# Kernel tuning notes

Measured on AMD Instinct MI355X. Metric: run time of the kernel, lower is better.

Reference implementation:

```python
import jax, jax.numpy as jnp
import numpy as np

VOCAB, D, K = 100000, 300, 5

def setup_inputs() -> dict:
    key = jax.random.key(0)
    ks = jax.random.split(key, 12)
    B, BAG, L = 64, 16, 128
    token_ids = jax.random.randint(ks[0], (B * BAG, L), 0, VOCAB)
    mention_rep = jax.random.normal(ks[1], (B, BAG, D), dtype=jnp.float32)
    s = 0.05
    emb = jax.random.normal(ks[2], (VOCAB, D), dtype=jnp.float32)
    W1 = jax.random.normal(ks[3], (D, D), dtype=jnp.float32) * s
    b1 = jnp.zeros((D,), jnp.float32)
    conv_w = jax.random.normal(ks[4], (D, D, K), dtype=jnp.float32) * s  # [out, in, k]
    conv_b = jnp.zeros((D,), jnp.float32)
    W2 = jax.random.normal(ks[5], (2 * D, D), dtype=jnp.float32) * s
    b2 = jnp.zeros((D,), jnp.float32)
    W3 = jax.random.normal(ks[6], (D, D), dtype=jnp.float32) * s
    b3 = jnp.zeros((D,), jnp.float32)
    return {"token_ids": token_ids, "mention_rep": mention_rep, "emb": emb,
            "W1": W1, "b1": b1, "conv_w": conv_w, "conv_b": conv_b,
            "W2": W2, "b2": b2, "W3": W3, "b3": b3}

def reference(token_ids, mention_rep, emb, W1, b1, conv_w, conv_b, W2, b2, W3, b3):
    # fused gather+pad: [N, L, D]
    x = emb[token_ids]
    # lin1
    x = x @ W1 + b1
    # conv1d over time, VALID, stride 1: NCH layout
    xc = jnp.transpose(x, (0, 2, 1))  # [N, D, L]
    y = jax.lax.conv_general_dilated(xc, conv_w, (1,), 'VALID',
                                     dimension_numbers=('NCH', 'OIH', 'NCH'))
    y = y + conv_b[None, :, None]
    cnn_out = jnp.max(y, axis=-1)  # [N, D]
    m = mention_rep.reshape(mention_rep.shape[0] * mention_rep.shape[1], -1)  # dropout = identity (eval)
    concat = jnp.concatenate([cnn_out, m], axis=-1)
    h = jnp.tanh(concat @ W2 + b2)
    out = h @ W3 + b3  # dropout = identity (eval)
    return out
```

## Files before the change

### kernel.cpp

```cpp
#include <hip/hip_runtime.h>


#define DD   300
#define LL   128
#define TOUT 124
#define CH   16
#define XR   20
#define NSTG 8
#define BLK  320
#define KS     19
#define SLABP  6080
#define ROWP   20
#define WS_G1_OFF  0
#define WS_CV_OFF  194560
#define WS_NEEDED  1167360
#define NPH        114

typedef __attribute__((ext_vector_type(8))) _Float16 f16x8;
typedef __attribute__((ext_vector_type(4))) _Float16 f16x4;
typedef __attribute__((ext_vector_type(4))) float f32x4;
typedef __attribute__((ext_vector_type(16))) float f32x16;
typedef unsigned int   u32;
typedef unsigned short u16;
typedef __attribute__((ext_vector_type(4))) u32 u32x4;

__device__ __forceinline__ float b2f(u16 u) {
    union { float f; u32 i; } x; x.i = ((u32)u) << 16; return x.f;
}
__device__ __forceinline__ u16 f2bu(float f) {
    union { float f; u32 i; } x; x.f = f;
    u32 r = x.i + 0x7FFFu + ((x.i >> 16) & 1u);
    return (u16)(r >> 16);
}
__device__ __forceinline__ float ld(const void* p, size_t idx, int is32) {
    return is32 ? ((const float*)p)[idx] : b2f(((const u16*)p)[idx]);
}
__device__ __forceinline__ int sniff_is32(const void* W1) {
    int cnt = 0;
    const u32* w1raw = (const u32*)W1;
    for (int i = 0; i < 64; ++i) {
        u32 e = (w1raw[i] >> 7) & 0xFFu;
        cnt += (e >= 100u && e <= 126u) ? 1 : 0;
    }
    return (cnt < 32) ? 1 : 0;
}

__device__ __forceinline__ void barrier_lgkm() {
    asm volatile("s_waitcnt lgkmcnt(0)" ::: "memory");
    __builtin_amdgcn_s_barrier();
}

__device__ __forceinline__ void unit_decomp(int u, int& o, int& kq) {
    kq = (u >= 912) ? 3 : (u >= 608) ? 2 : (u >= 304) ? 1 : 0;
    o  = u - 304 * kq;
}
__device__ __forceinline__ void g1_load(const float* W1f, int kk, int o, int kq, float r[4]) {
    const int kbase = kk * 16 + kq * 4;
    #pragma unroll
    for (int j = 0; j < 4; ++j) {
        const int k = kbase + j;
        r[j] = (k < DD && o < DD) ? W1f[(size_t)k * DD + o] : 0.f;
    }
}
__device__ __forceinline__ void g1_write(_Float16* Ws, int o, int kq, const float r[4]) {
    f16x4 v;
    #pragma unroll
    for (int j = 0; j < 4; ++j) v[j] = (_Float16)r[j];
    *(f16x4*)&Ws[o * ROWP + (kq << 2)] = v;
}
__device__ __forceinline__ void cv_load(const float* CWf, int kk, int o, int kq, float r[20]) {
    const int kbase = kk * 16 + kq * 4;
    const bool ok = (o < DD) && (kbase < DD);
    const float4* src = (const float4*)(CWf + (size_t)o * 1500 + kk * 80 + kq * 20);
    #pragma unroll
    for (int i = 0; i < 5; ++i) {
        float4 t = ok ? src[i] : float4{0.f, 0.f, 0.f, 0.f};
        r[4*i] = t.x; r[4*i+1] = t.y; r[4*i+2] = t.z; r[4*i+3] = t.w;
    }
}
__device__ __forceinline__ void cv_write(_Float16* Ws, int o, int kq, const float r[20]) {
    #pragma unroll
    for (int s = 0; s < 5; ++s) {
        f16x4 v;
        #pragma unroll
        for (int j = 0; j < 4; ++j) v[j] = (_Float16)r[j * 5 + s];
        *(f16x4*)&Ws[s * SLABP + o * ROWP + (kq << 2)] = v;
    }
}

__global__ void CNNEncoder_36258113912977_xform(
    const void* W1, const void* conv_w, void* ws)
{
    if (!sniff_is32(W1)) return;
    const int kk = blockIdx.x, part = blockIdx.y, tid = threadIdx.x;

    if (part == 0) {
        const float* W1f = (const float*)W1;
        f16x8* dst = (f16x8*)((char*)ws + WS_G1_OFF) + (size_t)kk * 640;
        for (int g = tid; g < 640; g += 512) {
            const int kc = (g >= 320) ? 1 : 0;
            const int nn = g - kc * 320;
            f16x8 v;
            #pragma unroll
            for (int e = 0; e < 8; ++e) {
                const int k = kk * 16 + kc * 8 + e;
                v[e] = (_Float16)((k < DD && nn < DD) ? W1f[(size_t)k * DD + nn] : 0.f);
            }
            dst[g] = v;
        }
    } else {
        const int s = part - 1;
        const float* CWf = (const float*)conv_w;
        f16x8* dst = (f16x8*)((char*)ws + WS_CV_OFF) + (size_t)kk * 3200 + (size_t)s * 640;
        for (int g = tid; g < 640; g += 512) {
            const int kc = (g >= 320) ? 1 : 0;
            const int nn = g - kc * 320;
            f16x8 v;
            #pragma unroll
            for (int e = 0; e < 8; ++e) {
                const int k = kk * 16 + kc * 8 + e;
                v[e] = (_Float16)((k < DD && nn < DD)
                        ? CWf[(size_t)nn * 1500 + (size_t)k * 5 + s] : 0.f);
            }
            dst[g] = v;
        }
    }
}

#define STAGE_PH(P, Q, QX) do {                                             \
    const int wr_ = (P) + 5;                                                \
    if (wr_ < NPH) {                                                        \
        _Float16* d_ = &ring[(wr_ % 6) * 5120];                             \
        *(u32x4*)&d_[tid * 8] = Q;                                          \
        if (tid < 128) *(u32x4*)&d_[(512 + tid) * 8] = QX;                  \
    }                                                                       \
    const int lp_ = (P) + 7;                                                \
    if (lp_ < NPH) {                                                        \
        const u32x4* s_ = (const u32x4*)wsAll + (size_t)lp_ * 640;          \
        Q = s_[tid];                                                        \
        if (tid < 128) QX = s_[512 + tid];                                  \
    }                                                                       \
} while (0)

#define PH_BODY(P, SROW, KKC, Q, QX) do {                                   \
    STAGE_PH((P), Q, QX);                                                   \
    const int phys_ = (P) % 6;                                              \
    const int c_ = 2 * (KKC) + lh;                                          \
    const int row_ = mrow0 + l31 + (SROW);                                  \
    const f16x8 a_ = *(const f16x8*)&XB[row_ * 320 + ((c_ ^ (row_ & 7)) << 3)]; \
    __builtin_amdgcn_s_setprio(1);                                          \
    _Pragma("unroll")                                                       \
    for (int nt_ = 0; nt_ < 5; ++nt_) {                                     \
        const int nn_ = nbase + nt_ * 32 + l31;                             \
        const f16x8 b_ = *(const f16x8*)&ring[phys_ * 5120 + lh * 2560 + nn_ * 8]; \
        acc[nt_] = __builtin_amdgcn_mfma_f32_32x32x16_f16(a_, b_, acc[nt_], 0, 0, 0); \
    }                                                                       \
    __builtin_amdgcn_s_setprio(0);                                          \
    barrier_lgkm();                                                         \
} while (0)

#define PH_G1(KK, Q, QX)    PH_BODY((KK), 0, (KK), Q, QX)
#define PH_CV(KK, S, Q, QX) PH_BODY(19 + (KK) * 5 + (S), (S), (KK), Q, QX)

__global__ __launch_bounds__(512, 2) void CNNEncoder_36258113912977_kernel(
    const int* __restrict__ tok, const void* mention, const void* emb,
    const void* W1, const void* b1, const void* conv_w, const void* conv_b,
    const void* W2, const void* b2, const void* W3, const void* b3,
    void* out, const void* ws)
{
    if (!sniff_is32(W1)) return;

    __shared__ __align__(16) _Float16 XB[132 * 320];
    __shared__ __align__(16) _Float16 ring[6 * 5120];
    __shared__ float pmax4[4][320];
    __shared__ float cbuf[2 * DD];
    __shared__ float hbuf[DD];

    const int n = blockIdx.x, tid = threadIdx.x;
    const int w   = tid >> 6;
    const int l   = tid & 63;
    const int l31 = l & 31, lh = l >> 5;
    const int wm  = w >> 1;
    const int wn  = w & 1;
    const int nbase = wn * 160;
    const int mrow0 = wm * 32;
    const int* trow = tok + (size_t)n * LL;
    const void* wsAll = ws;

    u32x4 qE, qO, qEx, qOx;
    u32x4 pre[5], prex[5];

    #pragma unroll
    for (int pl = 0; pl < 5; ++pl) {
        const u32x4* s_ = (const u32x4*)wsAll + (size_t)pl * 640;
        pre[pl] = s_[tid];
        if (tid < 128) prex[pl] = s_[512 + tid];
    }
    { const u32x4* s_ = (const u32x4*)wsAll + (size_t)5 * 640;
      qE = s_[tid]; if (tid < 128) qEx = s_[512 + tid]; }
    { const u32x4* s_ = (const u32x4*)wsAll + (size_t)6 * 640;
      qO = s_[tid]; if (tid < 128) qOx = s_[512 + tid]; }

    for (int i = tid; i < 132 * 160; i += 512) ((u32*)XB)[i] = 0u;
    __syncthreads();

    {
        const int r = tid >> 2, q = tid & 3;
        const float* erow = (const float*)emb + (size_t)trow[r] * DD;
        for (int c = q; c < 38; c += 4) {
            f16x8 v;
            if (c < 37) {
                const float4 f0 = *(const float4*)(erow + 8 * c);
                const float4 f1 = *(const float4*)(erow + 8 * c + 4);
                v[0]=(_Float16)f0.x; v[1]=(_Float16)f0.y;
                v[2]=(_Float16)f0.z; v[3]=(_Float16)f0.w;
                v[4]=(_Float16)f1.x; v[5]=(_Float16)f1.y;
                v[6]=(_Float16)f1.z; v[7]=(_Float16)f1.w;
            } else {
                const float4 f0 = *(const float4*)(erow + 296);
                v[0]=(_Float16)f0.x; v[1]=(_Float16)f0.y;
                v[2]=(_Float16)f0.z; v[3]=(_Float16)f0.w;
                v[4]=(_Float16)0.f; v[5]=(_Float16)0.f;
                v[6]=(_Float16)0.f; v[7]=(_Float16)0.f;
            }
            const int p = c ^ (r & 7);
            *(f16x8*)&XB[r * 320 + (p << 3)] = v;
        }
    }

    #pragma unroll
    for (int pl = 0; pl < 5; ++pl) {
        *(u32x4*)&ring[pl * 5120 + tid * 8] = pre[pl];
        if (tid < 128) *(u32x4*)&ring[pl * 5120 + (512 + tid) * 8] = prex[pl];
    }
    __syncthreads();

    f32x16 acc[5];
    #pragma unroll
    for (int nt = 0; nt < 5; ++nt)
        #pragma unroll
        for (int j = 0; j < 16; ++j) acc[nt][j] = 0.f;

    for (int kk = 0; kk < 18; kk += 2) {
        PH_G1(kk,     qE, qEx);
        PH_G1(kk + 1, qO, qOx);
    }
    PH_G1(18, qE, qEx);

    {
        const float* b1f = (const float*)b1;
        #pragma unroll
        for (int nt = 0; nt < 5; ++nt) {
            const int col = nbase + nt * 32 + l31;
            const float bb = (col < DD) ? b1f[col] : 0.f;
            const int cc = col >> 3, c7 = col & 7;
            #pragma unroll
            for (int q = 0; q < 4; ++q) {
                #pragma unroll
                for (int r = 0; r < 4; ++r) {
                    const int row = mrow0 + q * 8 + 4 * lh + r;
                    XB[row * 320 + ((cc ^ (row & 7)) << 3) + c7]
                        = (_Float16)(acc[nt][4 * q + r] + bb);
                }
            }
        }
    }
    __syncthreads();

    #pragma unroll
    for (int nt = 0; nt < 5; ++nt)
        #pragma unroll
        for (int j = 0; j < 16; ++j) acc[nt][j] = 0.f;

    for (int kk = 0; kk < 18; kk += 2) {
        PH_CV(kk, 0, qO, qOx);  PH_CV(kk, 1, qE, qEx);
        PH_CV(kk, 2, qO, qOx);  PH_CV(kk, 3, qE, qEx);
        PH_CV(kk, 4, qO, qOx);
        PH_CV(kk + 1, 0, qE, qEx);  PH_CV(kk + 1, 1, qO, qOx);
        PH_CV(kk + 1, 2, qE, qEx);  PH_CV(kk + 1, 3, qO, qOx);
        PH_CV(kk + 1, 4, qE, qEx);
    }
    PH_CV(18, 0, qO, qOx);  PH_CV(18, 1, qE, qEx);
    PH_CV(18, 2, qO, qOx);  PH_CV(18, 3, qE, qEx);
    PH_CV(18, 4, qO, qOx);

    #pragma unroll
    for (int nt = 0; nt < 5; ++nt) {
        float m = -3.0e38f;
        #pragma unroll
        for (int q = 0; q < 4; ++q) {
            if (!(wm == 3 && q == 3)) {
                #pragma unroll
                for (int r = 0; r < 4; ++r) m = fmaxf(m, acc[nt][4 * q + r]);
            } else if (lh == 0) {
                #pragma unroll
                for (int r = 0; r < 4; ++r) m = fmaxf(m, acc[nt][12 + r]);
            }
        }
        m = fmaxf(m, __shfl_xor(m, 32));
        if (lh == 0) pmax4[wm][nbase + nt * 32 + l31] = m;
    }
    __syncthreads();

    if (tid < DD) {
        float m = fmaxf(fmaxf(pmax4[0][tid], pmax4[1][tid]),
                        fmaxf(pmax4[2][tid], pmax4[3][tid]));
        cbuf[tid]      = m + ((const float*)conv_b)[tid];
        cbuf[DD + tid] = ((const float*)mention)[(size_t)n * DD + tid];
    }
    __syncthreads();

    if (tid < DD) {
        const float* W2f = (const float*)W2;
        float a0 = 0.f, a1 = 0.f, a2 = 0.f, a3 = 0.f;
        for (int c = 0; c < 2 * DD; c += 4) {
            a0 += cbuf[c]     * W2f[(size_t)c * DD + tid];
            a1 += cbuf[c + 1] * W2f[(size_t)(c + 1) * DD + tid];
            a2 += cbuf[c + 2] * W2f[(size_t)(c + 2) * DD + tid];
            a3 += cbuf[c + 3] * W2f[(size_t)(c + 3) * DD + tid];
        }
        hbuf[tid] = tanhf(((const float*)b2)[tid] + (a0 + a1) + (a2 + a3));
    }
    __syncthreads();

    if (tid < DD) {
        const float* W3f = (const float*)W3;
        float a0 = 0.f, a1 = 0.f;
        for (int c = 0; c < DD; c += 2) {
            a0 += hbuf[c]     * W3f[(size_t)c * DD + tid];
            a1 += hbuf[c + 1] * W3f[(size_t)(c + 1) * DD + tid];
        }
        ((float*)out)[(size_t)n * DD + tid] = ((const float*)b3)[tid] + a0 + a1;
    }
}

__global__ __launch_bounds__(512, 2) void CNNEncoder_36258113912977_nows(
    const int* __restrict__ tok, const void* mention, const void* emb,
    const void* W1, const void* b1, const void* conv_w, const void* conv_b,
    const void* W2, const void* b2, const void* W3, const void* b3,
    void* out)
{
    if (!sniff_is32(W1)) return;

    __shared__ __align__(16) _Float16 XB[132 * 320];
    __shared__ __align__(16) _Float16 Ws[5 * SLABP];
    __shared__ float pmax2[2][304];
    __shared__ float cbuf[2 * DD];
    __shared__ float hbuf[DD];

    const int n = blockIdx.x, tid = threadIdx.x;
    const int w   = tid >> 6;
    const int l   = tid & 63;
    const int l15 = l & 15, lg = l >> 4;
    const int wm  = w >> 2;
    const int wn  = w & 3;
    const int ntw   = (wn < 3) ? 5 : 4;
    const int nbase = wn * 80;
    const int mrow0 = wm * 64;
    const int* trow = tok + (size_t)n * LL;
    const float* W1f = (const float*)W1;
    const float* CWf = (const float*)conv_w;

    int o0, kq0, o1, kq1, o2, kq2;
    unit_decomp(tid, o0, kq0);
    unit_decomp(512 + tid, o1, kq1);
    const bool act2 = (l < 24);
    unit_decomp(1024 + w * 24 + (l < 24 ? l : 0), o2, kq2);

    for (int i = tid; i < 132 * 160; i += 512) ((u32*)XB)[i] = 0u;
    __syncthreads();

    {
        const int r = tid >> 2, q = tid & 3;
        const float* erow = (const float*)emb + (size_t)trow[r] * DD;
        for (int c = q; c < 38; c += 4) {
            f16x8 v;
            if (c < 37) {
                const float4 f0 = *(const float4*)(erow + 8 * c);
                const float4 f1 = *(const float4*)(erow + 8 * c + 4);
                v[0]=(_Float16)f0.x; v[1]=(_Float16)f0.y;
                v[2]=(_Float16)f0.z; v[3]=(_Float16)f0.w;
                v[4]=(_Float16)f1.x; v[5]=(_Float16)f1.y;
                v[6]=(_Float16)f1.z; v[7]=(_Float16)f1.w;
            } else {
                const float4 f0 = *(const float4*)(erow + 296);
                v[0]=(_Float16)f0.x; v[1]=(_Float16)f0.y;
                v[2]=(_Float16)f0.z; v[3]=(_Float16)f0.w;
                v[4]=(_Float16)0.f; v[5]=(_Float16)0.f;
                v[6]=(_Float16)0.f; v[7]=(_Float16)0.f;
            }
            const int p = c ^ (r & 7);
            *(f16x8*)&XB[r * 320 + (p << 3)] = v;
        }
    }

    f32x4 acc[4][5];
    const f32x4 vzero = {0.f, 0.f, 0.f, 0.f};
    #pragma unroll
    for (int mt = 0; mt < 4; ++mt)
        #pragma unroll
        for (int nt = 0; nt < 5; ++nt) acc[mt][nt] = vzero;

    float g1a[4], g1b[4], g1c[4];
    float cfa[20], cfb[20], cfc[20];

    g1_load(W1f, 0, o0, kq0, g1a);
    g1_load(W1f, 0, o1, kq1, g1b);
    if (act2) g1_load(W1f, 0, o2, kq2, g1c);
    __syncthreads();

    for (int kk = 0; kk < KS; ++kk) {
        g1_write(Ws, o0, kq0, g1a);
        g1_write(Ws, o1, kq1, g1b);
        if (act2) g1_write(Ws, o2, kq2, g1c);
        barrier_lgkm();
        if (kk + 1 < KS) {
            g1_load(W1f, kk + 1, o0, kq0, g1a);
            g1_load(W1f, kk + 1, o1, kq1, g1b);
            if (act2) g1_load(W1f, kk + 1, o2, kq2, g1c);
        } else {
            cv_load(CWf, 0, o0, kq0, cfa);
            cv_load(CWf, 0, o1, kq1, cfb);
            if (act2) cv_load(CWf, 0, o2, kq2, cfc);
        }
        {
            f16x4 af[4];
            #pragma unroll
            for (int mt = 0; mt < 4; ++mt) {
                const int row = mrow0 + mt * 16 + l15;
                const int c = (kk << 1) + (lg >> 1);
                af[mt] = *(const f16x4*)&XB[row * 320 + ((c ^ (row & 7)) << 3) + ((lg & 1) << 2)];
            }
            #pragma unroll
            for (int nt = 0; nt < 5; ++nt) {
                if (nt < ntw) {
                    const int nn = nbase + nt * 16 + l15;
                    const f16x4 b = *(const f16x4*)&Ws[nn * ROWP + (lg << 2)];
                    #pragma unroll
                    for (int mt = 0; mt < 4; ++mt)
                        acc[mt][nt] = __builtin_amdgcn_mfma_f32_16x16x16f16(af[mt], b, acc[mt][nt], 0, 0, 0);
                }
            }
        }
        __builtin_amdgcn_s_barrier();
    }

    {
        const float* b1f = (const float*)b1;
        #pragma unroll
        for (int nt = 0; nt < 5; ++nt) {
            if (nt < ntw) {
                const int col = nbase + nt * 16 + l15;
                const float bb = (col < DD) ? b1f[col] : 0.f;
                #pragma unroll
                for (int mt = 0; mt < 4; ++mt) {
                    #pragma unroll
                    for (int j = 0; j < 4; ++j) {
                        const int row = mrow0 + mt * 16 + (lg << 2) + j;
                        XB[row * 320 + (((col >> 3) ^ (row & 7)) << 3) + (col & 7)]
                            = (_Float16)(acc[mt][nt][j] + bb);
                    }
                }
            }
        }
    }

    #pragma unroll
    for (int mt = 0; mt < 4; ++mt)
        #pragma unroll
        for (int nt = 0; nt < 5; ++nt) acc[mt][nt] = vzero;

    for (int kk = 0; kk < KS; ++kk) {
        cv_write(Ws, o0, kq0, cfa);
        cv_write(Ws, o1, kq1, cfb);
        if (act2) cv_write(Ws, o2, kq2, cfc);
        barrier_lgkm();
        if (kk + 1 < KS) {
            cv_load(CWf, kk + 1, o0, kq0, cfa);
            cv_load(CWf, kk + 1, o1, kq1, cfb);
            if (act2) cv_load(CWf, kk + 1, o2, kq2, cfc);
        }
        #pragma unroll
        for (int s = 0; s < 5; ++s) {
            f16x4 af[4];
            #pragma unroll
            for (int mt = 0; mt < 4; ++mt) {
                const int row = mrow0 + mt * 16 + l15 + s;
                const int c = (kk << 1) + (lg >> 1);
                af[mt] = *(const f16x4*)&XB[row * 320 + ((c ^ (row & 7)) << 3) + ((lg & 1) << 2)];
            }
            #pragma unroll
            for (int nt = 0; nt < 5; ++nt) {
                if (nt < ntw) {
                    const int nn = nbase + nt * 16 + l15;
                    const f16x4 b = *(const f16x4*)&Ws[s * SLABP + nn * ROWP + (lg << 2)];
                    #pragma unroll
                    for (int mt = 0; mt < 4; ++mt)
                        acc[mt][nt] = __builtin_amdgcn_mfma_f32_16x16x16f16(af[mt], b, acc[mt][nt], 0, 0, 0);
                }
            }
        }
        __builtin_amdgcn_s_barrier();
    }

    #pragma unroll
    for (int nt = 0; nt < 5; ++nt) {
        if (nt < ntw) {
            float m = -3.0e38f;
            #pragma unroll
            for (int mt = 0; mt < 4; ++mt) {
                #pragma unroll
                for (int j = 0; j < 4; ++j) {
                    const int t = mrow0 + mt * 16 + (lg << 2) + j;
                    if (t < TOUT) m = fmaxf(m, acc[mt][nt][j]);
                }
            }
            m = fmaxf(m, __shfl_xor(m, 16));
            m = fmaxf(m, __shfl_xor(m, 32));
            if (lg == 0) pmax2[wm][nbase + nt * 16 + l15] = m;
        }
    }
    __syncthreads();

    if (tid < DD) {
        const float m = fmaxf(pmax2[0][tid], pmax2[1][tid]);
        cbuf[tid]      = m + ((const float*)conv_b)[tid];
        cbuf[DD + tid] = ((const float*)mention)[(size_t)n * DD + tid];
    }
    __syncthreads();

    if (tid < DD) {
        const float* W2f = (const float*)W2;
        float a0 = 0.f, a1 = 0.f, a2 = 0.f, a3 = 0.f;
        for (int c = 0; c < 2 * DD; c += 4) {
            a0 += cbuf[c]     * W2f[(size_t)c * DD + tid];
            a1 += cbuf[c + 1] * W2f[(size_t)(c + 1) * DD + tid];
            a2 += cbuf[c + 2] * W2f[(size_t)(c + 2) * DD + tid];
            a3 += cbuf[c + 3] * W2f[(size_t)(c + 3) * DD + tid];
        }
        hbuf[tid] = tanhf(((const float*)b2)[tid] + (a0 + a1) + (a2 + a3));
    }
    __syncthreads();

    if (tid < DD) {
        const float* W3f = (const float*)W3;
        float a0 = 0.f, a1 = 0.f;
        for (int c = 0; c < DD; c += 2) {
            a0 += hbuf[c]     * W3f[(size_t)c * DD + tid];
            a1 += hbuf[c + 1] * W3f[(size_t)(c + 1) * DD + tid];
        }
        ((float*)out)[(size_t)n * DD + tid] = ((const float*)b3)[tid] + a0 + a1;
    }
}

__global__ void CNNEncoder_36258113912977_fallback(
    const int* tok, const void* mention, const void* emb,
    const void* W1, const void* b1, const void* conv_w, const void* conv_b,
    const void* W2, const void* b2, const void* W3, const void* b3,
    void* out)
{
    __shared__ float g[XR * DD];
    __shared__ float xh[XR * DD];
    __shared__ float concat[2 * DD];
    __shared__ float hbuf[DD];

    const int n = blockIdx.x, tid = threadIdx.x;
    const int* trow = tok + (size_t)n * LL;

    if (sniff_is32(W1)) return;
    const int is32 = 0;

    float mmax = -3.0e38f;

    for (int stage = 0; stage < NSTG; ++stage) {
        const int tbase = stage * CH;
        __syncthreads();

        for (int i = tid; i < XR * DD; i += BLK) {
            int r = i / DD, c = i - (i / DD) * DD;
            int gr = tbase + r; if (gr > 127) gr = 127;
            g[i] = ld(emb, (size_t)trow[gr] * DD + c, is32);
        }
        __syncthreads();

        if (tid < DD) {
            float acc[XR];
            #pragma unroll
            for (int r = 0; r < XR; ++r) acc[r] = 0.f;
            for (int k = 0; k < DD; ++k) {
                float wv = ld(W1, (size_t)k * DD + tid, is32);
                #pragma unroll
                for (int r = 0; r < XR; ++r) acc[r] += g[r * DD + k] * wv;
            }
            float bb = ld(b1, tid, is32);
            #pragma unroll
            for (int r = 0; r < XR; ++r) xh[r * DD + tid] = acc[r] + bb;
        }
        __syncthreads();

        if (tid < DD) {
            float y[CH];
            #pragma unroll
            for (int t = 0; t < CH; ++t) y[t] = 0.f;
            const size_t cwoff = (size_t)tid * (DD * 5);
            for (int k = 0; k < DD; ++k) {
                #pragma unroll
                for (int s = 0; s < 5; ++s) {
                    float wv = ld(conv_w, cwoff + k * 5 + s, is32);
                    #pragma unroll
                    for (int t = 0; t < CH; ++t)
                        y[t] += xh[(t + s) * DD + k] * wv;
                }
            }
            #pragma unroll
            for (int t = 0; t < CH; ++t) {
                int tt = tbase + t;
                if (tt < TOUT) mmax = fmaxf(mmax, y[t]);
            }
        }
    }

    __syncthreads();
    if (tid < DD) {
        concat[tid]      = mmax + ld(conv_b, tid, is32);
        concat[DD + tid] = ld(mention, (size_t)n * DD + tid, is32);
    }
    __syncthreads();

    if (tid < DD) {
        float a = ld(b2, tid, is32);
        for (int c = 0; c < 2 * DD; ++c)
            a += concat[c] * ld(W2, (size_t)c * DD + tid, is32);
        hbuf[tid] = tanhf(a);
    }
    __syncthreads();

    if (tid < DD) {
        float a = ld(b3, tid, is32);
        for (int c = 0; c < DD; ++c)
            a += hbuf[c] * ld(W3, (size_t)c * DD + tid, is32);
        ((u16*)out)[(size_t)n * DD + tid] = f2bu(a);
    }
}

extern "C" void kernel_launch(void* const* d_in, const int* in_sizes, int n_in,
                              void* d_out, int out_size, void* d_ws, size_t ws_size,
                              hipStream_t stream)
{
    if (ws_size >= (size_t)WS_NEEDED && d_ws != nullptr) {
        CNNEncoder_36258113912977_xform<<<dim3(19, 6), 512, 0, stream>>>(
            d_in[3], d_in[5], d_ws);
        CNNEncoder_36258113912977_kernel<<<1024, 512, 0, stream>>>(
            (const int*)d_in[0], d_in[1], d_in[2], d_in[3], d_in[4], d_in[5],
            d_in[6], d_in[7], d_in[8], d_in[9], d_in[10], d_out, d_ws);
    } else {
        CNNEncoder_36258113912977_nows<<<1024, 512, 0, stream>>>(
            (const int*)d_in[0], d_in[1], d_in[2], d_in[3], d_in[4], d_in[5],
            d_in[6], d_in[7], d_in[8], d_in[9], d_in[10], d_out);
    }
    CNNEncoder_36258113912977_fallback<<<1024, BLK, 0, stream>>>(
        (const int*)d_in[0], d_in[1], d_in[2], d_in[3], d_in[4], d_in[5],
        d_in[6], d_in[7], d_in[8], d_in[9], d_in[10], d_out);
}
```

Before: 466.7 us.

## Double main kernel block to 1024 threads, splitting MFMA N-tiles across 16 waves

Each block of the main fused kernel now runs 16 waves instead of 8. Each wave owns two or three 32-wide N tiles instead of five, and ten waves together stage one full 640-vector weight phase into the LDS ring with one load each, so the extra tail loads are gone. The W2 and W3 epilogue matvecs are split into two partial sums over 600 threads and combined through a new shared buffer. The aim is more latency hiding and MFMA issue parallelism per CU while LDS limits residency to one block. The cost is lower per-wave accumulator reuse of the A operand, and a tighter register budget under the new launch bounds that may cause spills.

```diff
diff --git a/kernel.cpp b/kernel.cpp
--- a/kernel.cpp
+++ b/kernel.cpp
@@ -127,42 +127,65 @@
     }
 }
 
-#define STAGE_PH(P, Q, QX) do {                                             \
-    const int wr_ = (P) + 5;                                                \
-    if (wr_ < NPH) {                                                        \
-        _Float16* d_ = &ring[(wr_ % 6) * 5120];                             \
-        *(u32x4*)&d_[tid * 8] = Q;                                          \
-        if (tid < 128) *(u32x4*)&d_[(512 + tid) * 8] = QX;                  \
-    }                                                                       \
-    const int lp_ = (P) + 7;                                                \
-    if (lp_ < NPH) {                                                        \
-        const u32x4* s_ = (const u32x4*)wsAll + (size_t)lp_ * 640;          \
-        Q = s_[tid];                                                        \
-        if (tid < 128) QX = s_[512 + tid];                                  \
+#define STAGE_PH(P, Q) do {                                                 \
+    if (stager) {                                                           \
+        const int wr_ = (P) + 5;                                            \
+        if (wr_ < NPH) *(u32x4*)&ring[(wr_ % 6) * 5120 + sg * 8] = Q;       \
+        const int lp_ = (P) + 7;                                            \
+        if (lp_ < NPH) Q = ((const u32x4*)ws)[(size_t)lp_ * 640 + sg];      \
     }                                                                       \
 } while (0)
 
-#define PH_BODY(P, SROW, KKC, Q, QX) do {                                   \
-    STAGE_PH((P), Q, QX);                                                   \
-    const int phys_ = (P) % 6;                                              \
+#define PH_BODY(P, SROW, KKC, Q) do {                                       \
+    STAGE_PH((P), Q);                                                       \
     const int c_ = 2 * (KKC) + lh;                                          \
     const int row_ = mrow0 + l31 + (SROW);                                  \
     const f16x8 a_ = *(const f16x8*)&XB[row_ * 320 + ((c_ ^ (row_ & 7)) << 3)]; \
+    const _Float16* bp_ = &ring[((P) % 6) * 5120 + lh * 2560];              \
     __builtin_amdgcn_s_setprio(1);                                          \
-    _Pragma("unroll")                                                       \
-    for (int nt_ = 0; nt_ < 5; ++nt_) {                                     \
-        const int nn_ = nbase + nt_ * 32 + l31;                             \
-        const f16x8 b_ = *(const f16x8*)&ring[phys_ * 5120 + lh * 2560 + nn_ * 8]; \
-        acc[nt_] = __builtin_amdgcn_mfma_f32_32x32x16_f16(a_, b_, acc[nt_], 0, 0, 0); \
-    }                                                                       \
+    { const f16x8 b_ = *(const f16x8*)&bp_[nn0 * 8];                        \
+      acc0 = __builtin_amdgcn_mfma_f32_32x32x16_f16(a_, b_, acc0, 0, 0, 0); } \
+    { const f16x8 b_ = *(const f16x8*)&bp_[nn1 * 8];                        \
+      acc1 = __builtin_amdgcn_mfma_f32_32x32x16_f16(a_, b_, acc1, 0, 0, 0); } \
+    if (nt3) { const f16x8 b_ = *(const f16x8*)&bp_[nn2 * 8];               \
+      acc2 = __builtin_amdgcn_mfma_f32_32x32x16_f16(a_, b_, acc2, 0, 0, 0); } \
     __builtin_amdgcn_s_setprio(0);                                          \
     barrier_lgkm();                                                         \
 } while (0)
 
-#define PH_G1(KK, Q, QX)    PH_BODY((KK), 0, (KK), Q, QX)
-#define PH_CV(KK, S, Q, QX) PH_BODY(19 + (KK) * 5 + (S), (S), (KK), Q, QX)
-
-__global__ __launch_bounds__(512, 2) void CNNEncoder_36258113912977_kernel(
+#define PH_G1(KK, Q)    PH_BODY((KK), 0, (KK), Q)
+#define PH_CV(KK, S, Q) PH_BODY(19 + (KK) * 5 + (S), (S), (KK), Q)
+
+#define EPI_TILE(ACC, TILE) do {                                            \
+    const int col_ = (TILE) * 32 + l31;                                     \
+    const float bb_ = (col_ < DD) ? b1f[col_] : 0.f;                        \
+    const int cc_ = col_ >> 3, c7_ = col_ & 7;                              \
+    _Pragma("unroll")                                                       \
+    for (int q_ = 0; q_ < 4; ++q_) {                                        \
+        _Pragma("unroll")                                                   \
+        for (int r_ = 0; r_ < 4; ++r_) {                                    \
+            const int row_ = mrow0 + q_ * 8 + 4 * lh + r_;                  \
+            XB[row_ * 320 + ((cc_ ^ (row_ & 7)) << 3) + c7_]                \
+                = (_Float16)(ACC[4 * q_ + r_] + bb_);                       \
+        } }                                                                 \
+} while (0)
+
+#define MAX_TILE(ACC, TILE) do {                                            \
+    float m_ = -3.0e38f;                                                    \
+    _Pragma("unroll")                                                       \
+    for (int q_ = 0; q_ < 4; ++q_) {                                        \
+        if (!(wm == 3 && q_ == 3)) {                                        \
+            _Pragma("unroll")                                               \
+            for (int r_ = 0; r_ < 4; ++r_) m_ = fmaxf(m_, ACC[4 * q_ + r_]); \
+        } else if (lh == 0) {                                               \
+            _Pragma("unroll")                                               \
+            for (int r_ = 0; r_ < 4; ++r_) m_ = fmaxf(m_, ACC[12 + r_]);    \
+        } }                                                                 \
+    m_ = fmaxf(m_, __shfl_xor(m_, 32));                                     \
+    if (lh == 0) pmax4[wm][(TILE) * 32 + l31] = m_;                         \
+} while (0)
+
+__global__ __launch_bounds__(1024, 4) void CNNEncoder_36258113912977_kernel(
     const int* __restrict__ tok, const void* mention, const void* emb,
     const void* W1, const void* b1, const void* conv_w, const void* conv_b,
     const void* W2, const void* b2, const void* W3, const void* b3,
@@ -174,32 +197,187 @@
     __shared__ __align__(16) _Float16 ring[6 * 5120];
     __shared__ float pmax4[4][320];
     __shared__ float cbuf[2 * DD];
+    __shared__ float hpart[2][DD];
     __shared__ float hbuf[DD];
 
     const int n = blockIdx.x, tid = threadIdx.x;
     const int w   = tid >> 6;
     const int l   = tid & 63;
     const int l31 = l & 31, lh = l >> 5;
-    const int wm  = w >> 1;
-    const int wn  = w & 1;
-    const int nbase = wn * 160;
+    const int wm  = w >> 2;
+    const int wn  = w & 3;
     const int mrow0 = wm * 32;
+    const bool nt3 = (wn < 2);
+    const int nn0 = wn * 32 + l31;
+    const int nn1 = nn0 + 128;
+    const int nn2 = nn0 + 256;
+    const bool stager = (w < 10);
+    const int sg = w * 64 + l;
     const int* trow = tok + (size_t)n * LL;
-    const void* wsAll = ws;
-
-    u32x4 qE, qO, qEx, qOx;
-    u32x4 pre[5], prex[5];
-
-    #pragma unroll
-    for (int pl = 0; pl < 5; ++pl) {
-        const u32x4* s_ = (const u32x4*)wsAll + (size_t)pl * 640;
-        pre[pl] = s_[tid];
-        if (tid < 128) prex[pl] = s_[512 + tid];
-    }
-    { const u32x4* s_ = (const u32x4*)wsAll + (size_t)5 * 640;
-      qE = s_[tid]; if (tid < 128) qEx = s_[512 + tid]; }
-    { const u32x4* s_ = (const u32x4*)wsAll + (size_t)6 * 640;
-      qO = s_[tid]; if (tid < 128) qOx = s_[512 + tid]; }
+
+    u32x4 qE, qO;
+    u32x4 pre0, pre1, pre2, pre3, pre4;
+
+    if (stager) {
+        const u32x4* wsv = (const u32x4*)ws;
+        pre0 = wsv[sg];          pre1 = wsv[640 + sg];
+        pre2 = wsv[1280 + sg];   pre3 = wsv[1920 + sg];
+        pre4 = wsv[2560 + sg];
+        qE   = wsv[3200 + sg];
+        qO   = wsv[3840 + sg];
+    }
+
+    for (int i = tid; i < 132 * 160; i += 1024) ((u32*)XB)[i] = 0u;
+    barrier_lgkm();
+
+    {
+        const int r = tid >> 3, q = tid & 7;
+        const float* erow = (const float*)emb + (size_t)trow[r] * DD;
+        for (int c = q; c < 38; c += 8) {
+            f16x8 v;
+            if (c < 37) {
+                const float4 f0 = *(const float4*)(erow + 8 * c);
+                const float4 f1 = *(const float4*)(erow + 8 * c + 4);
+                v[0]=(_Float16)f0.x; v[1]=(_Float16)f0.y;
+                v[2]=(_Float16)f0.z; v[3]=(_Float16)f0.w;
+                v[4]=(_Float16)f1.x; v[5]=(_Float16)f1.y;
+                v[6]=(_Float16)f1.z; v[7]=(_Float16)f1.w;
+            } else {
+                const float4 f0 = *(const float4*)(erow + 296);
+                v[0]=(_Float16)f0.x; v[1]=(_Float16)f0.y;
+                v[2]=(_Float16)f0.z; v[3]=(_Float16)f0.w;
+                v[4]=(_Float16)0.f; v[5]=(_Float16)0.f;
+                v[6]=(_Float16)0.f; v[7]=(_Float16)0.f;
+            }
+            const int p = c ^ (r & 7);
+            *(f16x8*)&XB[r * 320 + (p << 3)] = v;
+        }
+    }
+
+    if (stager) {
+        *(u32x4*)&ring[0 * 5120 + sg * 8] = pre0;
+        *(u32x4*)&ring[1 * 5120 + sg * 8] = pre1;
+        *(u32x4*)&ring[2 * 5120 + sg * 8] = pre2;
+        *(u32x4*)&ring[3 * 5120 + sg * 8] = pre3;
+        *(u32x4*)&ring[4 * 5120 + sg * 8] = pre4;
+    }
+    barrier_lgkm();
+
+    f32x16 acc0, acc1, acc2;
+    #pragma unroll
+    for (int j = 0; j < 16; ++j) { acc0[j] = 0.f; acc1[j] = 0.f; acc2[j] = 0.f; }
+
+    for (int kk = 0; kk < 18; kk += 2) {
+        PH_G1(kk,     qE);
+        PH_G1(kk + 1, qO);
+    }
+    PH_G1(18, qE);
+
+    {
+        const float* b1f = (const float*)b1;
+        EPI_TILE(acc0, wn);
+        EPI_TILE(acc1, wn + 4);
+        if (nt3) EPI_TILE(acc2, wn + 8);
+    }
+    barrier_lgkm();
+
+    #pragma unroll
+    for (int j = 0; j < 16; ++j) { acc0[j] = 0.f; acc1[j] = 0.f; acc2[j] = 0.f; }
+
+    for (int kk = 0; kk < 18; kk += 2) {
+        PH_CV(kk, 0, qO);  PH_CV(kk, 1, qE);
+        PH_CV(kk, 2, qO);  PH_CV(kk, 3, qE);
+        PH_CV(kk, 4, qO);
+        PH_CV(kk + 1, 0, qE);  PH_CV(kk + 1, 1, qO);
+        PH_CV(kk + 1, 2, qE);  PH_CV(kk + 1, 3, qO);
+        PH_CV(kk + 1, 4, qE);
+    }
+    PH_CV(18, 0, qO);  PH_CV(18, 1, qE);
+    PH_CV(18, 2, qO);  PH_CV(18, 3, qE);
+    PH_CV(18, 4, qO);
+
+    MAX_TILE(acc0, wn);
+    MAX_TILE(acc1, wn + 4);
+    if (nt3) MAX_TILE(acc2, wn + 8);
+    __syncthreads();
+
+    if (tid < DD) {
+        float m = fmaxf(fmaxf(pmax4[0][tid], pmax4[1][tid]),
+                        fmaxf(pmax4[2][tid], pmax4[3][tid]));
+        cbuf[tid]      = m + ((const float*)conv_b)[tid];
+        cbuf[DD + tid] = ((const float*)mention)[(size_t)n * DD + tid];
+    }
+    __syncthreads();
+
+    if (tid < 2 * DD) {
+        const int part = (tid >= DD) ? 1 : 0;
+        const int j = tid - part * DD;
+        const float* W2f = (const float*)W2;
+        const int c0 = part * DD;
+        float a0 = 0.f, a1 = 0.f, a2 = 0.f, a3 = 0.f;
+        for (int c = c0; c < c0 + DD; c += 4) {
+            a0 += cbuf[c]     * W2f[(size_t)c * DD + j];
+            a1 += cbuf[c + 1] * W2f[(size_t)(c + 1) * DD + j];
+            a2 += cbuf[c + 2] * W2f[(size_t)(c + 2) * DD + j];
+            a3 += cbuf[c + 3] * W2f[(size_t)(c + 3) * DD + j];
+        }
+        hpart[part][j] = (a0 + a1) + (a2 + a3);
+    }
+    __syncthreads();
+    if (tid < DD)
+        hbuf[tid] = tanhf(((const float*)b2)[tid] + hpart[0][tid] + hpart[1][tid]);
+    __syncthreads();
+
+    if (tid < 2 * DD) {
+        const int part = (tid >= DD) ? 1 : 0;
+        const int j = tid - part * DD;
+        const float* W3f = (const float*)W3;
+        const int c0 = part * 150;
+        float a0 = 0.f, a1 = 0.f;
+        for (int c = c0; c < c0 + 150; c += 2) {
+            a0 += hbuf[c]     * W3f[(size_t)c * DD + j];
+            a1 += hbuf[c + 1] * W3f[(size_t)(c + 1) * DD + j];
+        }
+        hpart[part][j] = a0 + a1;
+    }
+    __syncthreads();
+    if (tid < DD)
+        ((float*)out)[(size_t)n * DD + tid]
+            = ((const float*)b3)[tid] + hpart[0][tid] + hpart[1][tid];
+}
+
+__global__ __launch_bounds__(512, 2) void CNNEncoder_36258113912977_nows(
+    const int* __restrict__ tok, const void* mention, const void* emb,
+    const void* W1, const void* b1, const void* conv_w, const void* conv_b,
+    const void* W2, const void* b2, const void* W3, const void* b3,
+    void* out)
+{
+    if (!sniff_is32(W1)) return;
+
+    __shared__ __align__(16) _Float16 XB[132 * 320];
+    __shared__ __align__(16) _Float16 Ws[5 * SLABP];
+    __shared__ float pmax2[2][304];
+    __shared__ float cbuf[2 * DD];
+    __shared__ float hbuf[DD];
+
+    const int n = blockIdx.x, tid = threadIdx.x;
+    const int w   = tid >> 6;
+    const int l   = tid & 63;
+    const int l15 = l & 15, lg = l >> 4;
+    const int wm  = w >> 2;
+    const int wn  = w & 3;
+    const int ntw   = (wn < 3) ? 5 : 4;
+    const int nbase = wn * 80;
+    const int mrow0 = wm * 64;
+    const int* trow = tok + (size_t)n * LL;
+    const float* W1f = (const float*)W1;
+    const float* CWf = (const float*)conv_w;
+
+    int o0, kq0, o1, kq1, o2, kq2;
+    unit_decomp(tid, o0, kq0);
+    unit_decomp(512 + tid, o1, kq1);
+    const bool act2 = (l < 24);
+    unit_decomp(1024 + w * 24 + (l < 24 ? l : 0), o2, kq2);
 
     for (int i = tid; i < 132 * 160; i += 512) ((u32*)XB)[i] = 0u;
     __syncthreads();
@@ -228,172 +406,6 @@
         }
     }
 
-    #pragma unroll
-    for (int pl = 0; pl < 5; ++pl) {
-        *(u32x4*)&ring[pl * 5120 + tid * 8] = pre[pl];
-        if (tid < 128) *(u32x4*)&ring[pl * 5120 + (512 + tid) * 8] = prex[pl];
-    }
-    __syncthreads();
-
-    f32x16 acc[5];
-    #pragma unroll
-    for (int nt = 0; nt < 5; ++nt)
-        #pragma unroll
-        for (int j = 0; j < 16; ++j) acc[nt][j] = 0.f;
-
-    for (int kk = 0; kk < 18; kk += 2) {
-        PH_G1(kk,     qE, qEx);
-        PH_G1(kk + 1, qO, qOx);
-    }
-    PH_G1(18, qE, qEx);
-
-    {
-        const float* b1f = (const float*)b1;
-        #pragma unroll
-        for (int nt = 0; nt < 5; ++nt) {
-            const int col = nbase + nt * 32 + l31;
-            const float bb = (col < DD) ? b1f[col] : 0.f;
-            const int cc = col >> 3, c7 = col & 7;
-            #pragma unroll
-            for (int q = 0; q < 4; ++q) {
-                #pragma unroll
-                for (int r = 0; r < 4; ++r) {
-                    const int row = mrow0 + q * 8 + 4 * lh + r;
-                    XB[row * 320 + ((cc ^ (row & 7)) << 3) + c7]
-                        = (_Float16)(acc[nt][4 * q + r] + bb);
-                }
-            }
-        }
-    }
-    __syncthreads();
-
-    #pragma unroll
-    for (int nt = 0; nt < 5; ++nt)
-        #pragma unroll
-        for (int j = 0; j < 16; ++j) acc[nt][j] = 0.f;
-
-    for (int kk = 0; kk < 18; kk += 2) {
-        PH_CV(kk, 0, qO, qOx);  PH_CV(kk, 1, qE, qEx);
-        PH_CV(kk, 2, qO, qOx);  PH_CV(kk, 3, qE, qEx);
-        PH_CV(kk, 4, qO, qOx);
-        PH_CV(kk + 1, 0, qE, qEx);  PH_CV(kk + 1, 1, qO, qOx);
-        PH_CV(kk + 1, 2, qE, qEx);  PH_CV(kk + 1, 3, qO, qOx);
-        PH_CV(kk + 1, 4, qE, qEx);
-    }
-    PH_CV(18, 0, qO, qOx);  PH_CV(18, 1, qE, qEx);
-    PH_CV(18, 2, qO, qOx);  PH_CV(18, 3, qE, qEx);
-    PH_CV(18, 4, qO, qOx);
-
-    #pragma unroll
-    for (int nt = 0; nt < 5; ++nt) {
-        float m = -3.0e38f;
-        #pragma unroll
-        for (int q = 0; q < 4; ++q) {
-            if (!(wm == 3 && q == 3)) {
-                #pragma unroll
-                for (int r = 0; r < 4; ++r) m = fmaxf(m, acc[nt][4 * q + r]);
-            } else if (lh == 0) {
-                #pragma unroll
-                for (int r = 0; r < 4; ++r) m = fmaxf(m, acc[nt][12 + r]);
-            }
-        }
-        m = fmaxf(m, __shfl_xor(m, 32));
-        if (lh == 0) pmax4[wm][nbase + nt * 32 + l31] = m;
-    }
-    __syncthreads();
-
-    if (tid < DD) {
-        float m = fmaxf(fmaxf(pmax4[0][tid], pmax4[1][tid]),
-                        fmaxf(pmax4[2][tid], pmax4[3][tid]));
-        cbuf[tid]      = m + ((const float*)conv_b)[tid];
-        cbuf[DD + tid] = ((const float*)mention)[(size_t)n * DD + tid];
-    }
-    __syncthreads();
-
-    if (tid < DD) {
-        const float* W2f = (const float*)W2;
-        float a0 = 0.f, a1 = 0.f, a2 = 0.f, a3 = 0.f;
-        for (int c = 0; c < 2 * DD; c += 4) {
-            a0 += cbuf[c]     * W2f[(size_t)c * DD + tid];
-            a1 += cbuf[c + 1] * W2f[(size_t)(c + 1) * DD + tid];
-            a2 += cbuf[c + 2] * W2f[(size_t)(c + 2) * DD + tid];
-            a3 += cbuf[c + 3] * W2f[(size_t)(c + 3) * DD + tid];
-        }
-        hbuf[tid] = tanhf(((const float*)b2)[tid] + (a0 + a1) + (a2 + a3));
-    }
-    __syncthreads();
-
-    if (tid < DD) {
-        const float* W3f = (const float*)W3;
-        float a0 = 0.f, a1 = 0.f;
-        for (int c = 0; c < DD; c += 2) {
-            a0 += hbuf[c]     * W3f[(size_t)c * DD + tid];
-            a1 += hbuf[c + 1] * W3f[(size_t)(c + 1) * DD + tid];
-        }
-        ((float*)out)[(size_t)n * DD + tid] = ((const float*)b3)[tid] + a0 + a1;
-    }
-}
-
-__global__ __launch_bounds__(512, 2) void CNNEncoder_36258113912977_nows(
-    const int* __restrict__ tok, const void* mention, const void* emb,
-    const void* W1, const void* b1, const void* conv_w, const void* conv_b,
-    const void* W2, const void* b2, const void* W3, const void* b3,
-    void* out)
-{
-    if (!sniff_is32(W1)) return;
-
-    __shared__ __align__(16) _Float16 XB[132 * 320];
-    __shared__ __align__(16) _Float16 Ws[5 * SLABP];
-    __shared__ float pmax2[2][304];
-    __shared__ float cbuf[2 * DD];
-    __shared__ float hbuf[DD];
-
-    const int n = blockIdx.x, tid = threadIdx.x;
-    const int w   = tid >> 6;
-    const int l   = tid & 63;
-    const int l15 = l & 15, lg = l >> 4;
-    const int wm  = w >> 2;
-    const int wn  = w & 3;
-    const int ntw   = (wn < 3) ? 5 : 4;
-    const int nbase = wn * 80;
-    const int mrow0 = wm * 64;
-    const int* trow = tok + (size_t)n * LL;
-    const float* W1f = (const float*)W1;
-    const float* CWf = (const float*)conv_w;
-
-    int o0, kq0, o1, kq1, o2, kq2;
-    unit_decomp(tid, o0, kq0);
-    unit_decomp(512 + tid, o1, kq1);
-    const bool act2 = (l < 24);
-    unit_decomp(1024 + w * 24 + (l < 24 ? l : 0), o2, kq2);
-
-    for (int i = tid; i < 132 * 160; i += 512) ((u32*)XB)[i] = 0u;
-    __syncthreads();
-
-    {
-        const int r = tid >> 2, q = tid & 3;
-        const float* erow = (const float*)emb + (size_t)trow[r] * DD;
-        for (int c = q; c < 38; c += 4) {
-            f16x8 v;
-            if (c < 37) {
-                const float4 f0 = *(const float4*)(erow + 8 * c);
-                const float4 f1 = *(const float4*)(erow + 8 * c + 4);
-                v[0]=(_Float16)f0.x; v[1]=(_Float16)f0.y;
-                v[2]=(_Float16)f0.z; v[3]=(_Float16)f0.w;
-                v[4]=(_Float16)f1.x; v[5]=(_Float16)f1.y;
-                v[6]=(_Float16)f1.z; v[7]=(_Float16)f1.w;
-            } else {
-                const float4 f0 = *(const float4*)(erow + 296);
-                v[0]=(_Float16)f0.x; v[1]=(_Float16)f0.y;
-                v[2]=(_Float16)f0.z; v[3]=(_Float16)f0.w;
-                v[4]=(_Float16)0.f; v[5]=(_Float16)0.f;
-                v[6]=(_Float16)0.f; v[7]=(_Float16)0.f;
-            }
-            const int p = c ^ (r & 7);
-            *(f16x8*)&XB[r * 320 + (p << 3)] = v;
-        }
-    }
-
     f32x4 acc[4][5];
     const f32x4 vzero = {0.f, 0.f, 0.f, 0.f};
     #pragma unroll
@@ -650,7 +662,7 @@
     if (ws_size >= (size_t)WS_NEEDED && d_ws != nullptr) {
         CNNEncoder_36258113912977_xform<<<dim3(19, 6), 512, 0, stream>>>(
             d_in[3], d_in[5], d_ws);
-        CNNEncoder_36258113912977_kernel<<<1024, 512, 0, stream>>>(
+        CNNEncoder_36258113912977_kernel<<<1024, 1024, 0, stream>>>(
             (const int*)d_in[0], d_in[1], d_in[2], d_in[3], d_in[4], d_in[5],
             d_in[6], d_in[7], d_in[8], d_in[9], d_in[10], d_out, d_ws);
     } else {
```

Result: slower. 520.0 us (+11.4%).
